# Kernel tuning notes

Measured on AMD Instinct MI355X. Metric: run time of the kernel, lower is better.

## Reference

```python
import jax, jax.numpy as jnp
import numpy as np


def setup_inputs() -> dict:
    key = jax.random.key(0)
    k1, k2, k3, k4 = jax.random.split(key, 4)
    B, S, D, H = 64, 512, 1024, 1024
    scale = 1.0 / np.sqrt(H)
    x = jax.random.normal(k1, (B, S, D), dtype=jnp.float32)
    Wx = jax.random.normal(k2, (D, H), dtype=jnp.float32) * scale
    Wh = jax.random.normal(k3, (H, H), dtype=jnp.float32) * scale
    b = jax.random.normal(k4, (H,), dtype=jnp.float32) * scale
    return {"x": x, "Wx": Wx, "Wh": Wh, "b": b}


def reference(x, Wx, Wh, b):
    # Elman tanh RNN cell: h_t = tanh(x_t @ Wx + h_{t-1} @ Wh + b)
    # Truncated BPTT: carried state is detached each step (stop_gradient),
    # matching `state = state.detach()` in the torch forward.
    B, S, D = x.shape
    H = Wh.shape[0]
    h0 = jnp.zeros((B, H), dtype=x.dtype)  # get_initial_state
    # precompute input projections for all timesteps: [S, B, H]
    xw = jnp.swapaxes(jnp.einsum('bsd,dh->bsh', x, Wx) + b, 0, 1)

    def step(h_prev, xw_t):
        h_new = jnp.tanh(xw_t + h_prev @ Wh)
        return jax.lax.stop_gradient(h_new), h_new

    _, hs = jax.lax.scan(step, h0, xw)  # hs: [S, B, H]
    return jnp.swapaxes(hs, 0, 1)  # [B, S, H]
```

## Files before the change

### kernel.cpp

```cpp
#include <hip/hip_runtime.h>
#include <stdint.h>

#define B_  64
#define S_  512
#define D_  1024
#define H_  1024

#define NBLK2 128

typedef __attribute__((ext_vector_type(2))) float    f32x2;
typedef __attribute__((ext_vector_type(4))) float    f32x4;
typedef __attribute__((ext_vector_type(4))) uint32_t u32x4;
typedef __attribute__((ext_vector_type(8))) __bf16   bf16x8;

__device__ __forceinline__ f32x4 mfma16(bf16x8 a, bf16x8 b, f32x4 c) {
  return __builtin_amdgcn_mfma_f32_16x16x32_bf16(a, b, c, 0, 0, 0);
}

__device__ __forceinline__ void gload_lds16(const void* g, void* l) {
  __builtin_amdgcn_global_load_lds(
      (const __attribute__((address_space(1))) void*)g,
      (__attribute__((address_space(3))) void*)l, 16, 0, 0);
}

__device__ __forceinline__ void st_dword_sc(uint32_t* p, uint32_t v) {
  asm volatile("global_store_dword %0, %1, off sc0 sc1" :: "v"(p), "v"(v) : "memory");
}
__device__ __forceinline__ void ld_dwordx4_sc_issue(u32x4& dst, const void* p) {
  asm volatile("global_load_dwordx4 %0, %1, off sc0 sc1" : "=v"(dst) : "v"(p));
}

__device__ __forceinline__ uint32_t permhi(uint32_t a, uint32_t b) {
  return __builtin_amdgcn_perm(a, b, 0x07060302u);
}

__device__ __forceinline__ float tanh_fast(float x) {
  float ax = fabsf(x);
  float e = __expf(-2.0f * ax);
  float r = (1.0f - e) / (1.0f + e);
  return x < 0.0f ? -r : r;
}

__device__ __forceinline__ void split8(f32x4 a0, f32x4 a1, bf16x8& hi, bf16x8& lo) {
  float f[8] = {a0.x, a0.y, a0.z, a0.w, a1.x, a1.y, a1.z, a1.w};
  uint32_t hb[8], lb[8];
#pragma unroll
  for (int i = 0; i < 8; ++i) {
    uint32_t b = __builtin_bit_cast(uint32_t, f[i]);
    hb[i] = b;
    float hf = __builtin_bit_cast(float, b & 0xffff0000u);
    lb[i] = __builtin_bit_cast(uint32_t, f[i] - hf);
  }
  u32x4 hv = {permhi(hb[1], hb[0]), permhi(hb[3], hb[2]),
              permhi(hb[5], hb[4]), permhi(hb[7], hb[6])};
  u32x4 lv = {permhi(lb[1], lb[0]), permhi(lb[3], lb[2]),
              permhi(lb[5], lb[4]), permhi(lb[7], lb[6])};
  hi = __builtin_bit_cast(bf16x8, hv);
  lo = __builtin_bit_cast(bf16x8, lv);
}

__global__ __launch_bounds__(256) void prep_kernel(
    const float* __restrict__ Wx, const float* __restrict__ Wh,
    uint16_t* __restrict__ wxt_hi, uint16_t* __restrict__ wxt_lo,
    uint16_t* __restrict__ wht_hi, uint16_t* __restrict__ wht_lo,
    uint32_t* __restrict__ hq)
{
  {
    int gid = blockIdx.x * 256 + threadIdx.x;
    if (gid < 2 * 64 * 1024) hq[gid] = 0xFFFFFFFFu;
  }
  __shared__ float tile[32][33];
  int bid = blockIdx.x;
  int mat = bid >> 10;
  int t   = bid & 1023;
  int tk = t >> 5, tn = t & 31;
  const float* src = mat ? Wh : Wx;
  uint16_t* dhi = mat ? wht_hi : wxt_hi;
  uint16_t* dlo = mat ? wht_lo : wxt_lo;
  int tx = threadIdx.x & 31, ty0 = threadIdx.x >> 5;
  int k0 = tk * 32, n0 = tn * 32;
#pragma unroll
  for (int i = 0; i < 4; ++i) {
    int ty = ty0 + 8 * i;
    tile[ty][tx] = src[(size_t)(k0 + ty) * 1024 + n0 + tx];
  }
  __syncthreads();
#pragma unroll
  for (int i = 0; i < 4; ++i) {
    int ty = ty0 + 8 * i;
    float v = tile[tx][ty];
    uint32_t bv = __builtin_bit_cast(uint32_t, v);
    float lo = v - __builtin_bit_cast(float, bv & 0xffff0000u);
    uint32_t lbv = __builtin_bit_cast(uint32_t, lo);
    size_t o = (size_t)(n0 + ty) * 1024 + k0 + tx;
    dhi[o] = (uint16_t)(bv >> 16);
    dlo[o] = (uint16_t)(lbv >> 16);
  }
}

__global__ __launch_bounds__(256) void xw_gemm_kernel(
    const float* __restrict__ x, const uint16_t* __restrict__ wxt_hi,
    const uint16_t* __restrict__ wxt_lo, const float* __restrict__ bias,
    float* __restrict__ out)
{
  __shared__ __align__(16) float    ldsA[128 * 32];
  __shared__ __align__(16) uint16_t ldsBh[128 * 32];
  __shared__ __align__(16) uint16_t ldsBl[128 * 32];

  int bid = blockIdx.x;
  int swz = (bid & 7) * 256 + (bid >> 3);
  int mt = swz >> 3, nt = swz & 7;
  int M0 = mt * 128, N0 = nt * 128;

  int tid = threadIdx.x;
  int w = tid >> 6, l = tid & 63;
  int wm = w >> 1, wn = w & 1;

  int a_row = l >> 3;
  int a_sw  = ((l & 7) ^ (l >> 3)) << 4;
  int b_row = l >> 2;
  int b_sw  = (((l & 3) ^ ((l >> 2) & 3)) << 4);

  f32x4 acc[4][4];
#pragma unroll
  for (int i = 0; i < 4; ++i)
#pragma unroll
    for (int j = 0; j < 4; ++j) acc[i][j] = (f32x4){0.f, 0.f, 0.f, 0.f};

  const char* xb  = (const char*)x;
  const char* bhp = (const char*)wxt_hi;
  const char* blp = (const char*)wxt_lo;

  for (int s = 0; s < 32; ++s) {
#pragma unroll
    for (int j = 0; j < 4; ++j) {
      int i = 4 * w + j;
      const char* g = xb + ((size_t)(M0 + 8 * i + a_row) * 4096) + s * 128 + a_sw;
      gload_lds16(g, (char*)ldsA + i * 1024);
    }
#pragma unroll
    for (int j = 0; j < 2; ++j) {
      int i = 2 * w + j;
      size_t ro = (size_t)(N0 + 16 * i + b_row) * 2048 + s * 64 + b_sw;
      gload_lds16(bhp + ro, (char*)ldsBh + i * 1024);
      gload_lds16(blp + ro, (char*)ldsBl + i * 1024);
    }
    __syncthreads();

    bf16x8 ah[4], al[4], bh[4], bl[4];
#pragma unroll
    for (int mi = 0; mi < 4; ++mi) {
      int row = 64 * wm + 16 * mi + (l & 15);
      int kb  = (l >> 4) * 32;
      int sw  = (row & 7) << 4;
      f32x4 a0 = *(const f32x4*)((const char*)ldsA + row * 128 + (kb ^ sw));
      f32x4 a1 = *(const f32x4*)((const char*)ldsA + row * 128 + ((kb + 16) ^ sw));
      split8(a0, a1, ah[mi], al[mi]);
    }
#pragma unroll
    for (int ni = 0; ni < 4; ++ni) {
      int n  = 64 * wn + 16 * ni + (l & 15);
      int kb = (l >> 4) * 16;
      int off = n * 64 + (kb ^ ((n & 3) << 4));
      bh[ni] = *(const bf16x8*)((const char*)ldsBh + off);
      bl[ni] = *(const bf16x8*)((const char*)ldsBl + off);
    }
#pragma unroll
    for (int mi = 0; mi < 4; ++mi)
#pragma unroll
      for (int ni = 0; ni < 4; ++ni) {
        acc[mi][ni] = mfma16(ah[mi], bh[ni], acc[mi][ni]);
        acc[mi][ni] = mfma16(al[mi], bh[ni], acc[mi][ni]);
        acc[mi][ni] = mfma16(ah[mi], bl[ni], acc[mi][ni]);
      }
    __syncthreads();
  }

#pragma unroll
  for (int ni = 0; ni < 4; ++ni) {
    int col = N0 + 64 * wn + 16 * ni + (l & 15);
    float bv = bias[col];
#pragma unroll
    for (int mi = 0; mi < 4; ++mi) {
      int row0 = M0 + 64 * wm + 16 * mi + 4 * (l >> 4);
#pragma unroll
      for (int r = 0; r < 4; ++r)
        out[(size_t)(row0 + r) * 1024 + col] = acc[mi][ni][r] + bv;
    }
  }
}

__global__ __launch_bounds__(512, 1) void rnn_seq_kernel(
    float* __restrict__ out,
    const uint16_t* wht_hi, const uint16_t* wht_lo,
    uint32_t* __restrict__ hq)
{
  __shared__ __align__(16) float red[2][8][16][33];

  const int bid = blockIdx.x;
  const int g   = bid >> 5;
  const int c   = bid & 31;
  const int c0  = c * 32;

  const int tid = threadIdx.x;
  const int kw  = tid >> 6;
  const int l   = tid & 63;
  const int lr  = l & 15, lq = l >> 4;

  u32x4 wbh[2][4], wbl[2][4];
#pragma unroll
  for (int n2 = 0; n2 < 2; ++n2) {
    const size_t colb = (size_t)(c0 + n2 * 16 + lr) * 1024 + kw * 128 + lq * 8;
#pragma unroll
    for (int kc = 0; kc < 4; ++kc) {
      wbh[n2][kc] = *(const u32x4*)(wht_hi + colb + kc * 32);
      wbl[n2][kc] = *(const u32x4*)(wht_lo + colb + kc * 32);
    }
  }

  const uint32_t* hq_base = hq + (size_t)(g * 16 + lr) * 1024 + kw * 128 + lq * 8;
  const int HQ = 64 * 1024;

  const int frow = tid >> 5;
  const int fcol = tid & 31;
  const size_t out_base = ((size_t)(g * 16 + frow) * 512) * 1024 + c0 + fcol;
  const size_t h_off    = (size_t)(g * 16 + frow) * 1024 + c0 + fcol;

  for (int t = 0; t < 512; ++t) {
#pragma unroll
    for (int n2 = 0; n2 < 2; ++n2)
#pragma unroll
      for (int kc = 0; kc < 4; ++kc) {
        asm volatile("" : "+v"(wbh[n2][kc]));
        asm volatile("" : "+v"(wbl[n2][kc]));
      }

    float xwv = out[out_base + (size_t)t * 1024];

    f32x4 cH0 = {0.f,0.f,0.f,0.f}, cL0 = {0.f,0.f,0.f,0.f};
    f32x4 cH1 = {0.f,0.f,0.f,0.f}, cL1 = {0.f,0.f,0.f,0.f};

    if (t > 0) {
      const uint32_t* hb = hq_base + ((t - 1) & 1) * HQ;
      const uint32_t expect = (uint32_t)(t - 1) & 0xffffu;
      u32x4 pk[4][2];
      while (true) {
#pragma unroll
        for (int kc = 0; kc < 4; ++kc) {
          ld_dwordx4_sc_issue(pk[kc][0], hb + kc * 32);
          ld_dwordx4_sc_issue(pk[kc][1], hb + kc * 32 + 4);
        }
        __builtin_amdgcn_sched_barrier(0);
        asm volatile("s_waitcnt vmcnt(0)" ::: "memory");
        __builtin_amdgcn_sched_barrier(0);
        uint32_t bad = 0;
#pragma unroll
        for (int kc = 0; kc < 4; ++kc)
#pragma unroll
          for (int j = 0; j < 2; ++j)
#pragma unroll
            for (int e = 0; e < 4; ++e)
              bad |= (pk[kc][j][e] ^ expect);
        bad &= 0xffffu;
        if (!__any((int)bad)) break;
        __builtin_amdgcn_s_sleep(1);
      }
#pragma unroll
      for (int kc = 0; kc < 4; ++kc) {
        u32x4 aw;
        aw[0] = permhi(pk[kc][0][1], pk[kc][0][0]);
        aw[1] = permhi(pk[kc][0][3], pk[kc][0][2]);
        aw[2] = permhi(pk[kc][1][1], pk[kc][1][0]);
        aw[3] = permhi(pk[kc][1][3], pk[kc][1][2]);
        bf16x8 a = __builtin_bit_cast(bf16x8, aw);
        cH0 = mfma16(a, __builtin_bit_cast(bf16x8, wbh[0][kc]), cH0);
        cH1 = mfma16(a, __builtin_bit_cast(bf16x8, wbh[1][kc]), cH1);
        cL0 = mfma16(a, __builtin_bit_cast(bf16x8, wbl[0][kc]), cL0);
        cL1 = mfma16(a, __builtin_bit_cast(bf16x8, wbl[1][kc]), cL1);
      }
    }

    f32x4 acc0 = cH0 + cL0;
    f32x4 acc1 = cH1 + cL1;

    const int rbuf = t & 1;
#pragma unroll
    for (int r = 0; r < 4; ++r) {
      red[rbuf][kw][lq * 4 + r][lr]      = acc0[r];
      red[rbuf][kw][lq * 4 + r][16 + lr] = acc1[r];
    }
    __syncthreads();

    float s = 0.f;
#pragma unroll
    for (int wv = 0; wv < 8; ++wv)
      s += red[rbuf][wv][frow][fcol];

    float hval = tanh_fast(s + xwv);

    if (t < 511) {
      uint32_t b  = __builtin_bit_cast(uint32_t, hval);
      uint32_t hi = (b + 0x7fffu + ((b >> 16) & 1u)) & 0xffff0000u;
      st_dword_sc(hq + (size_t)(t & 1) * HQ + h_off, hi | (uint32_t)t);
    }
    out[out_base + (size_t)t * 1024] = hval;
  }
}

extern "C" void kernel_launch(void* const* d_in, const int* in_sizes, int n_in,
                              void* d_out, int out_size, void* d_ws, size_t ws_size,
                              hipStream_t stream) {
  const float* x    = (const float*)d_in[0];
  const float* Wx   = (const float*)d_in[1];
  const float* Wh   = (const float*)d_in[2];
  const float* bias = (const float*)d_in[3];
  float* out = (float*)d_out;

  char* ws = (char*)d_ws;
  uint16_t* wxt_hi = (uint16_t*)(ws);
  uint16_t* wxt_lo = (uint16_t*)(ws + (2u << 20));
  uint16_t* wht_hi = (uint16_t*)(ws + (4u << 20));
  uint16_t* wht_lo = (uint16_t*)(ws + (6u << 20));
  uint32_t* hq     = (uint32_t*)(ws + (8u << 20));

  prep_kernel<<<dim3(2048), dim3(256), 0, stream>>>(Wx, Wh, wxt_hi, wxt_lo,
                                                    wht_hi, wht_lo, hq);
  xw_gemm_kernel<<<dim3(2048), dim3(256), 0, stream>>>(x, wxt_hi, wxt_lo, bias, out);
  rnn_seq_kernel<<<dim3(NBLK2), dim3(512), 0, stream>>>(out, wht_hi, wht_lo, hq);
}
```

Before: 1.751 ms.

## Stage recurrent weights in swizzled LDS instead of holding them in registers

The prep kernel now writes the split hi/lo Wh tiles in a per-block, XOR-swizzled grouped layout. The sequential RNN kernel copies its 128 KB weight slice into LDS once with direct global-to-LDS loads, then re-reads the fragments from LDS every timestep rather than keeping them pinned in VGPRs. This frees registers that were previously locked by asm barriers. The cost is LDS reads on the serial critical path of each step, plus an extra __syncthreads per step, since the reduction buffer is now single-buffered.

```diff
diff --git a/kernel.cpp b/kernel.cpp
--- a/kernel.cpp
+++ b/kernel.cpp
@@ -62,8 +62,7 @@
 __global__ __launch_bounds__(256) void prep_kernel(
     const float* __restrict__ Wx, const float* __restrict__ Wh,
     uint16_t* __restrict__ wxt_hi, uint16_t* __restrict__ wxt_lo,
-    uint16_t* __restrict__ wht_hi, uint16_t* __restrict__ wht_lo,
-    uint32_t* __restrict__ hq)
+    uint16_t* __restrict__ whg, uint32_t* __restrict__ hq)
 {
   {
     int gid = blockIdx.x * 256 + threadIdx.x;
@@ -75,8 +74,6 @@
   int t   = bid & 1023;
   int tk = t >> 5, tn = t & 31;
   const float* src = mat ? Wh : Wx;
-  uint16_t* dhi = mat ? wht_hi : wxt_hi;
-  uint16_t* dlo = mat ? wht_lo : wxt_lo;
   int tx = threadIdx.x & 31, ty0 = threadIdx.x >> 5;
   int k0 = tk * 32, n0 = tn * 32;
 #pragma unroll
@@ -92,9 +89,20 @@
     uint32_t bv = __builtin_bit_cast(uint32_t, v);
     float lo = v - __builtin_bit_cast(float, bv & 0xffff0000u);
     uint32_t lbv = __builtin_bit_cast(uint32_t, lo);
-    size_t o = (size_t)(n0 + ty) * 1024 + k0 + tx;
-    dhi[o] = (uint16_t)(bv >> 16);
-    dlo[o] = (uint16_t)(lbv >> 16);
+    uint16_t hv16 = (uint16_t)(bv >> 16);
+    uint16_t lv16 = (uint16_t)(lbv >> 16);
+    int n = n0 + ty, k = k0 + tx;
+    if (!mat) {
+      size_t o = (size_t)n * 1024 + k;
+      wxt_hi[o] = hv16;
+      wxt_lo[o] = lv16;
+    } else {
+      int cb = n >> 5, cl = n & 31;
+      size_t base = (size_t)cb * 65536 + (size_t)cl * 1024
+                  + (size_t)(k ^ ((cl & 7) << 3));
+      whg[base]         = hv16;
+      whg[base + 32768] = lv16;
+    }
   }
 }
 
@@ -192,10 +200,11 @@
 
 __global__ __launch_bounds__(512, 1) void rnn_seq_kernel(
     float* __restrict__ out,
-    const uint16_t* wht_hi, const uint16_t* wht_lo,
+    const uint16_t* __restrict__ whg,
     uint32_t* __restrict__ hq)
 {
-  __shared__ __align__(16) float red[2][8][16][33];
+  __shared__ __align__(16) uint16_t whlds[2 * 32768];
+  __shared__ __align__(16) float red[8][16][33];
 
   const int bid = blockIdx.x;
   const int g   = bid >> 5;
@@ -207,19 +216,20 @@
   const int l   = tid & 63;
   const int lr  = l & 15, lq = l >> 4;
 
-  u32x4 wbh[2][4], wbl[2][4];
-#pragma unroll
-  for (int n2 = 0; n2 < 2; ++n2) {
-    const size_t colb = (size_t)(c0 + n2 * 16 + lr) * 1024 + kw * 128 + lq * 8;
-#pragma unroll
-    for (int kc = 0; kc < 4; ++kc) {
-      wbh[n2][kc] = *(const u32x4*)(wht_hi + colb + kc * 32);
-      wbl[n2][kc] = *(const u32x4*)(wht_lo + colb + kc * 32);
-    }
-  }
+  {
+    const char* src = (const char*)(whg + (size_t)c * 65536);
+#pragma unroll
+    for (int r = 0; r < 16; ++r)
+      gload_lds16(src + r * 8192 + tid * 16, (char*)whlds + r * 8192 + tid * 16);
+    asm volatile("s_waitcnt vmcnt(0)" ::: "memory");
+  }
+  __syncthreads();
 
   const uint32_t* hq_base = hq + (size_t)(g * 16 + lr) * 1024 + kw * 128 + lq * 8;
   const int HQ = 64 * 1024;
+
+  const int wsw = (lr & 7) << 4;
+  const int kbb = kw * 256 + lq * 16;
 
   const int frow = tid >> 5;
   const int fcol = tid & 31;
@@ -227,13 +237,16 @@
   const size_t h_off    = (size_t)(g * 16 + frow) * 1024 + c0 + fcol;
 
   for (int t = 0; t < 512; ++t) {
-#pragma unroll
-    for (int n2 = 0; n2 < 2; ++n2)
-#pragma unroll
-      for (int kc = 0; kc < 4; ++kc) {
-        asm volatile("" : "+v"(wbh[n2][kc]));
-        asm volatile("" : "+v"(wbl[n2][kc]));
-      }
+    u32x4 wb[2][2][4];
+#pragma unroll
+    for (int hf = 0; hf < 2; ++hf)
+#pragma unroll
+      for (int n2 = 0; n2 < 2; ++n2)
+#pragma unroll
+        for (int kc = 0; kc < 4; ++kc)
+          wb[hf][n2][kc] = *(const u32x4*)((const char*)whlds
+              + hf * 65536 + (n2 * 16 + lr) * 2048
+              + ((kbb + kc * 64) ^ wsw));
 
     float xwv = out[out_base + (size_t)t * 1024];
 
@@ -273,37 +286,37 @@
         aw[2] = permhi(pk[kc][1][1], pk[kc][1][0]);
         aw[3] = permhi(pk[kc][1][3], pk[kc][1][2]);
         bf16x8 a = __builtin_bit_cast(bf16x8, aw);
-        cH0 = mfma16(a, __builtin_bit_cast(bf16x8, wbh[0][kc]), cH0);
-        cH1 = mfma16(a, __builtin_bit_cast(bf16x8, wbh[1][kc]), cH1);
-        cL0 = mfma16(a, __builtin_bit_cast(bf16x8, wbl[0][kc]), cL0);
-        cL1 = mfma16(a, __builtin_bit_cast(bf16x8, wbl[1][kc]), cL1);
+        cH0 = mfma16(a, __builtin_bit_cast(bf16x8, wb[0][0][kc]), cH0);
+        cH1 = mfma16(a, __builtin_bit_cast(bf16x8, wb[0][1][kc]), cH1);
+        cL0 = mfma16(a, __builtin_bit_cast(bf16x8, wb[1][0][kc]), cL0);
+        cL1 = mfma16(a, __builtin_bit_cast(bf16x8, wb[1][1][kc]), cL1);
       }
     }
 
     f32x4 acc0 = cH0 + cL0;
     f32x4 acc1 = cH1 + cL1;
 
-    const int rbuf = t & 1;
 #pragma unroll
     for (int r = 0; r < 4; ++r) {
-      red[rbuf][kw][lq * 4 + r][lr]      = acc0[r];
-      red[rbuf][kw][lq * 4 + r][16 + lr] = acc1[r];
+      red[kw][lq * 4 + r][lr]      = acc0[r];
+      red[kw][lq * 4 + r][16 + lr] = acc1[r];
     }
     __syncthreads();
 
     float s = 0.f;
 #pragma unroll
     for (int wv = 0; wv < 8; ++wv)
-      s += red[rbuf][wv][frow][fcol];
+      s += red[wv][frow][fcol];
 
     float hval = tanh_fast(s + xwv);
-
     if (t < 511) {
       uint32_t b  = __builtin_bit_cast(uint32_t, hval);
       uint32_t hi = (b + 0x7fffu + ((b >> 16) & 1u)) & 0xffff0000u;
       st_dword_sc(hq + (size_t)(t & 1) * HQ + h_off, hi | (uint32_t)t);
     }
     out[out_base + (size_t)t * 1024] = hval;
+
+    __syncthreads();
   }
 }
 
@@ -319,12 +332,11 @@
   char* ws = (char*)d_ws;
   uint16_t* wxt_hi = (uint16_t*)(ws);
   uint16_t* wxt_lo = (uint16_t*)(ws + (2u << 20));
-  uint16_t* wht_hi = (uint16_t*)(ws + (4u << 20));
-  uint16_t* wht_lo = (uint16_t*)(ws + (6u << 20));
+  uint16_t* whg    = (uint16_t*)(ws + (4u << 20));
   uint32_t* hq     = (uint32_t*)(ws + (8u << 20));
 
   prep_kernel<<<dim3(2048), dim3(256), 0, stream>>>(Wx, Wh, wxt_hi, wxt_lo,
-                                                    wht_hi, wht_lo, hq);
+                                                    whg, hq);
   xw_gemm_kernel<<<dim3(2048), dim3(256), 0, stream>>>(x, wxt_hi, wxt_lo, bias, out);
-  rnn_seq_kernel<<<dim3(NBLK2), dim3(512), 0, stream>>>(out, wht_hi, wht_lo, hq);
-}
+  rnn_seq_kernel<<<dim3(NBLK2), dim3(512), 0, stream>>>(out, whg, hq);
+}
```

After: 1.918 ms. 1.1x slower.
